# Optimization experiments

Measured on AMD Instinct MI355X. Metric: run time of the kernel, lower is better.

Reference implementation:

```python
import jax, jax.numpy as jnp
import numpy as np

M = 1024      # num_inducing
B = 131072    # batch of query points (original module is per-query; we vmap/vectorize)
EPS_D = 1e-8
JITTER = 1e-4

Z_SCALE = np.array([0.15, 0.1, 0.05, 800.0, 20.0], dtype=np.float32)
Z_SHIFT = np.array([0.0, 0.0, 0.0, 600.0, 5.0], dtype=np.float32)


def setup_inputs() -> dict:
    key = jax.random.key(0)
    k1, k2 = jax.random.split(key)
    x_star = jax.random.normal(k1, (B, 5), dtype=jnp.float32)
    # learnable params, sized/initialized per the flax module
    log_lengthscale = jnp.log(jnp.array([0.2, 0.15, 0.1, 400.0, 15.0], dtype=jnp.float32))
    log_variance = jnp.asarray(jnp.log(0.08), dtype=jnp.float32)
    Z_raw = jax.random.uniform(k2, (M, 5), dtype=jnp.float32)  # uniform(scale=1.0) init
    return {"x_star": x_star, "log_lengthscale": log_lengthscale,
            "log_variance": log_variance, "Z_raw": Z_raw}


def _pairwise_sqdist(A, Bm):
    # ||a-b||^2 via gemm; A:(n,d), Bm:(m,d) -> (n,m)
    aa = jnp.sum(A * A, axis=-1)
    bb = jnp.sum(Bm * Bm, axis=-1)
    d2 = aa[:, None] + bb[None, :] - 2.0 * (A @ Bm.T)
    return jnp.maximum(d2, 0.0)


def _matern52(d2, prior_var):
    d = jnp.sqrt(d2 + EPS_D)
    s = jnp.sqrt(5.0) * d
    return prior_var * (1.0 + s + (5.0 / 3.0) * (d * d)) * jnp.exp(-s)


def reference(x_star, log_lengthscale, log_variance, Z_raw):
    ls = jnp.exp(log_lengthscale)                # (5,)
    prior_var = jnp.exp(log_variance)            # scalar
    Z = Z_raw * jnp.asarray(Z_SCALE) + jnp.asarray(Z_SHIFT)  # (M,5)
    inv_ls = 1.0 / (ls + 1e-8)
    Zs = Z * inv_ls                              # lengthscale-scaled inducing pts
    Xs = x_star * inv_ls                         # (B,5)

    K_ZZ = _matern52(_pairwise_sqdist(Zs, Zs), prior_var)            # (M,M)
    K_ZZ_inv = jnp.linalg.inv(K_ZZ + JITTER * jnp.eye(M, dtype=K_ZZ.dtype))

    k_xZ = _matern52(_pairwise_sqdist(Xs, Zs), prior_var)            # (B,M)
    red = jnp.sum(k_xZ * (k_xZ @ K_ZZ_inv), axis=-1)                 # (B,)
    variance = jnp.maximum(prior_var - red, 1e-6)
    return jnp.sqrt(variance)                                        # (B,) predictive std
```

## Files before the change

kernel.cpp:

```cpp
#include <hip/hip_runtime.h>
#include <math.h>

#define B_TOT 131072
#define M_N   1024
#define BS    128
#define NBK   8

typedef float  f32x4  __attribute__((ext_vector_type(4)));
typedef short  bf16x8 __attribute__((ext_vector_type(8)));

enum : size_t {
    OFF_K   = 0,
    OFF_WF  = (size_t)8 << 20,
    OFF_W11 = (size_t)12 << 20,
    OFF_PF  = (size_t)13 << 20,
    OFF_ZT  = ((size_t)13 << 20) + 256,
    OFF_WPH = (size_t)14 << 20,
    OFF_WPL = (size_t)16 << 20,
};

__device__ __constant__ double c_zscale[5] = {0.15, 0.1, 0.05, 800.0, 20.0};
__device__ __constant__ double c_zshift[5] = {0.0, 0.0, 0.0, 600.0, 5.0};

static __device__ __forceinline__ unsigned short f2bf(float f) {
    unsigned u = __float_as_uint(f);
    unsigned r = (u + 0x7fff + ((u >> 16) & 1)) >> 16;
    return (unsigned short)r;
}
static __device__ __forceinline__ float bf2f(unsigned short s) {
    return __uint_as_float(((unsigned)s) << 16);
}

__global__ __launch_bounds__(256) void k_build(const float* __restrict__ log_ls,
                                               const float* __restrict__ log_var,
                                               const float* __restrict__ Zraw,
                                               double* __restrict__ Kd,
                                               float* __restrict__ pf,
                                               float* __restrict__ Zst) {
    __shared__ double pd[6];
    __shared__ double zsi[5];
    int tid = threadIdx.x;
    if (tid < 5) pd[tid] = 1.0 / (exp((double)log_ls[tid]) + 1e-8);
    if (tid == 5) pd[5] = exp((double)log_var[0]);
    __syncthreads();
    int i = blockIdx.x >> 2;
    int j = (blockIdx.x & 3) * 256 + tid;
    if (tid < 5) zsi[tid] = ((double)Zraw[i * 5 + tid] * c_zscale[tid] + c_zshift[tid]) * pd[tid];
    __syncthreads();
    double d2 = 0.0;
#pragma unroll
    for (int d = 0; d < 5; ++d) {
        double zj = ((double)Zraw[j * 5 + d] * c_zscale[d] + c_zshift[d]) * pd[d];
        double df = zsi[d] - zj;
        d2 += df * df;
    }
    double dd = d2 + 1e-8;
    double dist = sqrt(dd);
    double s = 2.2360679774997896 * dist;
    double v = pd[5] * (1.0 + s + (5.0 / 3.0) * dd) * exp(-s);
    if (i == j) v += 1e-4;
    Kd[(size_t)i * M_N + j] = v;
    if (blockIdx.x < 4) {
        int m = blockIdx.x * 256 + tid;
#pragma unroll
        for (int d = 0; d < 5; ++d)
            Zst[d * M_N + m] = (float)(((double)Zraw[m * 5 + d] * c_zscale[d] + c_zshift[d]) * pd[d]);
    }
    if (blockIdx.x == 4 && tid < 6) pf[tid] = (float)pd[tid];
}

__global__ __launch_bounds__(512) void kw_diag(double* __restrict__ Kd,
                                               double* __restrict__ Wd11,
                                               float* __restrict__ Wf, int kb) {
    __shared__ double As[128][129];
    __shared__ double sinv[128];
    int tid = threadIdx.x;
    int r0 = kb * BS;
    for (int idx = tid; idx < BS * BS; idx += 512) {
        int rr = idx >> 7, cc = idx & 127;
        As[rr][cc] = Kd[(size_t)(r0 + rr) * M_N + r0 + cc];
    }
    __syncthreads();

    int r = tid & 127;
    int q = tid >> 7;
    for (int p = 0; p < 16; ++p) {
        int j0 = p * 8;
        for (int j = j0; j < j0 + 8; ++j) {
            if (tid == j) {
                double d = sqrt(As[j][j]);
                As[j][j] = d;
                sinv[j] = 1.0 / d;
            }
            __syncthreads();
            double arj = 0.0;
            if (q == 0 && r > j) {
                arj = As[r][j] * sinv[j];
                As[r][j] = arj;
            }
            __syncthreads();
            if (q == 0 && r > j) {
#pragma unroll
                for (int c = j + 1; c < j0 + 8; ++c)
                    As[r][c] -= arj * As[c][j];
            }
        }
        __syncthreads();
        if (p < 15) {
            double a[8];
#pragma unroll
            for (int t = 0; t < 8; ++t) a[t] = As[r][j0 + t];
            for (int c = j0 + 8 + q; c < 128; c += 4) {
                if (r >= c) {
                    double s = As[r][c];
#pragma unroll
                    for (int t = 0; t < 8; ++t) s -= a[t] * As[c][j0 + t];
                    As[r][c] = s;
                }
            }
        }
        __syncthreads();
    }

    if (tid < 128) {
        int c = tid;
        for (int rb = 0; rb < 16; ++rb) {
            int r0b = rb * 8;
            if (c >= r0b + 8) continue;
            double s[8];
#pragma unroll
            for (int i = 0; i < 8; ++i) s[i] = 0.0;
            for (int t = 0; t < r0b; ++t) {
                if (t >= c) {
                    double xt = (t == c) ? sinv[c] : As[c][t];
#pragma unroll
                    for (int i = 0; i < 8; ++i) s[i] += As[r0b + i][t] * xt;
                }
            }
            double xloc[8];
#pragma unroll
            for (int i = 0; i < 8; ++i) {
                int rr = r0b + i;
                double v = 0.0;
                if (rr >= c) {
                    v = ((rr == c) ? 1.0 : 0.0) - s[i];
#pragma unroll
                    for (int t2 = 0; t2 < i; ++t2) {
                        int tt = r0b + t2;
                        if (tt >= c) v -= As[rr][tt] * xloc[t2];
                    }
                    v *= sinv[rr];
                    if (rr > c) As[c][rr] = v;
                }
                xloc[i] = v;
            }
        }
    }
    __syncthreads();
    for (int idx = tid; idx < BS * BS; idx += 512) {
        int rr = idx >> 7, cc = idx & 127;
        if (rr >= cc) {
            double v = (rr == cc) ? sinv[rr] : As[cc][rr];
            Wd11[(size_t)kb * BS * BS + rr * BS + cc] = v;
            Wf[(size_t)(r0 + rr) * M_N + r0 + cc] = (float)v;
        }
    }
}

__global__ __launch_bounds__(256) void kw_panel(double* __restrict__ Kd,
                                                const double* __restrict__ Wd11, int kb) {
    __shared__ double As[64][16];
    __shared__ double Ws[16][128];
    int tid = threadIdx.x;
    int row0 = (kb + 1) * BS + blockIdx.x * 64;
    int cb = kb * BS;
    int c = tid & 127, q = tid >> 7;
    double acc[32];
#pragma unroll
    for (int i = 0; i < 32; ++i) acc[i] = 0.0;
    for (int tc = 0; tc < 8; ++tc) {
        int tb = tc * 16;
        for (int idx = tid; idx < 64 * 16; idx += 256) {
            int rr = idx >> 4, tt = idx & 15;
            As[rr][tt] = Kd[(size_t)(row0 + rr) * M_N + cb + tb + tt];
        }
        for (int idx = tid; idx < 128 * 16; idx += 256) {
            int cc = idx >> 4, tt = idx & 15;
            Ws[tt][cc] = (tb + tt <= cc) ? Wd11[(size_t)kb * BS * BS + cc * BS + tb + tt] : 0.0;
        }
        __syncthreads();
#pragma unroll
        for (int t = 0; t < 16; ++t) {
            double w = Ws[t][c];
#pragma unroll
            for (int i = 0; i < 32; ++i) acc[i] += As[q * 32 + i][t] * w;
        }
        __syncthreads();
    }
#pragma unroll
    for (int i = 0; i < 32; ++i)
        Kd[(size_t)(row0 + q * 32 + i) * M_N + cb + c] = acc[i];
}

__global__ __launch_bounds__(256) void kw_update(double* __restrict__ Kd, int kb) {
    __shared__ double As2[64][17];
    __shared__ double Bs2[64][17];
    int tid = threadIdx.x;
    int v = blockIdx.x;
    int by = 0;
    while ((by + 1) * (by + 2) / 2 <= v) ++by;
    int bx = v - by * (by + 1) / 2;
    int base = (kb + 1) * BS;
    int gr0 = base + by * 64;
    int gc0 = base + bx * 64;
    int cb = kb * BS;
    int tx = tid & 15, ty = tid >> 4;
    double acc[4][4];
#pragma unroll
    for (int i = 0; i < 4; ++i)
#pragma unroll
        for (int j = 0; j < 4; ++j) acc[i][j] = 0.0;
    for (int tc = 0; tc < 8; ++tc) {
        int tb = tc * 16;
        for (int idx = tid; idx < 1024; idx += 256) {
            int rr = idx >> 4, tt = idx & 15;
            As2[rr][tt] = Kd[(size_t)(gr0 + rr) * M_N + cb + tb + tt];
            Bs2[rr][tt] = Kd[(size_t)(gc0 + rr) * M_N + cb + tb + tt];
        }
        __syncthreads();
#pragma unroll
        for (int t = 0; t < 16; ++t) {
            double a[4], b[4];
#pragma unroll
            for (int i = 0; i < 4; ++i) a[i] = As2[ty * 4 + i][t];
#pragma unroll
            for (int j = 0; j < 4; ++j) b[j] = Bs2[tx * 4 + j][t];
#pragma unroll
            for (int i = 0; i < 4; ++i)
#pragma unroll
                for (int j = 0; j < 4; ++j) acc[i][j] += a[i] * b[j];
        }
        __syncthreads();
    }
#pragma unroll
    for (int i = 0; i < 4; ++i)
#pragma unroll
        for (int j = 0; j < 4; ++j)
            Kd[(size_t)(gr0 + ty * 4 + i) * M_N + gc0 + tx * 4 + j] -= acc[i][j];
}

__global__ __launch_bounds__(512) void kw_trtri(const double* __restrict__ Kd,
                                                float* __restrict__ Wf) {
    __shared__ float Ls[128][33];
    __shared__ float Ws[32][33];
    __shared__ float Whist[6][128][33];
    __shared__ float Ps[128][33];
    int j  = blockIdx.y;
    int ct = blockIdx.x;
    int c0 = j * BS + ct * 32;
    int tid = threadIdx.x;
    int rq = tid >> 2, cq = tid & 3;

    for (int i = j + 1; i < 8; ++i) {
        float acc[8];
#pragma unroll
        for (int c = 0; c < 8; ++c) acc[c] = 0.0f;
        for (int t = j; t < i; ++t) {
            for (int ch = 0; ch < 4; ++ch) {
                int tb = t * BS + ch * 32;
                __syncthreads();
                for (int idx = tid; idx < 128 * 32; idx += 512) {
                    int rr = idx >> 5, tt = idx & 31;
                    Ls[rr][tt] = (float)Kd[(size_t)(i * BS + rr) * M_N + tb + tt];
                }
                if (t == j) {
                    for (int idx = tid; idx < 32 * 32; idx += 512) {
                        int tt = idx >> 5, cc = idx & 31;
                        int gr = tb + tt, gc = c0 + cc;
                        Ws[tt][cc] = (gr >= gc) ? Wf[(size_t)gr * M_N + gc] : 0.0f;
                    }
                }
                __syncthreads();
                if (t == j) {
#pragma unroll
                    for (int tt = 0; tt < 32; ++tt) {
                        float l = Ls[rq][tt];
#pragma unroll
                        for (int c = 0; c < 8; ++c)
                            acc[c] = fmaf(l, Ws[tt][cq * 8 + c], acc[c]);
                    }
                } else {
                    const float (*Wh)[33] = Whist[t - j - 1];
#pragma unroll
                    for (int tt = 0; tt < 32; ++tt) {
                        float l = Ls[rq][tt];
#pragma unroll
                        for (int c = 0; c < 8; ++c)
                            acc[c] = fmaf(l, Wh[ch * 32 + tt][cq * 8 + c], acc[c]);
                    }
                }
            }
        }
        __syncthreads();
#pragma unroll
        for (int c = 0; c < 8; ++c) Ps[rq][cq * 8 + c] = acc[c];
        float a2[8];
#pragma unroll
        for (int c = 0; c < 8; ++c) a2[c] = 0.0f;
        for (int ch = 0; ch < 4; ++ch) {
            __syncthreads();
            for (int idx = tid; idx < 128 * 32; idx += 512) {
                int rr = idx >> 5, tt = idx & 31;
                Ls[rr][tt] = (rr >= ch * 32 + tt)
                           ? Wf[(size_t)(i * BS + rr) * M_N + i * BS + ch * 32 + tt] : 0.0f;
            }
            __syncthreads();
#pragma unroll
            for (int tt = 0; tt < 32; ++tt) {
                float l = Ls[rq][tt];
#pragma unroll
                for (int c = 0; c < 8; ++c)
                    a2[c] = fmaf(l, Ps[ch * 32 + tt][cq * 8 + c], a2[c]);
            }
        }
        __syncthreads();
#pragma unroll
        for (int c = 0; c < 8; ++c) {
            float v = -a2[c];
            Wf[(size_t)(i * BS + rq) * M_N + c0 + cq * 8 + c] = v;
            if (i < 7) Whist[i - j - 1][rq][cq * 8 + c] = v;
        }
        __syncthreads();
    }
}

__global__ void kw_pack(const float* __restrict__ Wf, short* __restrict__ Wph,
                        short* __restrict__ Wpl) {
    int T = blockIdx.x * 256 + threadIdx.x;
    int lane = T & 63, fid = T >> 6;
    int jn = fid & 63, kik = fid >> 6;
    int ki = kik & 3, kc = kik >> 2;
    int j  = jn * 16 + (lane & 15);
    int kb = kc * 128 + ki * 32 + (lane >> 4) * 8;
    bf16x8 h, lo;
#pragma unroll
    for (int e = 0; e < 8; ++e) {
        int k = kb + e;
        float v = (k <= j) ? Wf[(size_t)j * M_N + k] : 0.0f;
        unsigned short hb = f2bf(v);
        h[e]  = (short)hb;
        lo[e] = (short)f2bf(v - bf2f(hb));
    }
    size_t off = (size_t)fid * 512 + lane * 8;
    *(bf16x8*)(Wph + off) = h;
    *(bf16x8*)(Wpl + off) = lo;
}

__global__ __launch_bounds__(512, 1) void k_mm(const float* __restrict__ x_star,
                                               const float* __restrict__ pf,
                                               const float* __restrict__ Zs_t,
                                               const short* __restrict__ Wph,
                                               const short* __restrict__ Wpl,
                                               float* __restrict__ out, int Bq) {
    __shared__ __align__(16) char kls[2][32 * 256];
    __shared__ float red_l[32];
    int tid  = threadIdx.x;
    int slab = blockIdx.x;
    int w = tid >> 6, lane = tid & 63;
    int lrow = lane & 15, kgrp = lane >> 4;

    int srow = tid >> 4, scc = tid & 15;
    int qrow = slab * 32 + srow;
    int qc = (qrow < Bq) ? qrow : (Bq - 1);
    float xv0 = x_star[(size_t)qc * 5 + 0] * pf[0];
    float xv1 = x_star[(size_t)qc * 5 + 1] * pf[1];
    float xv2 = x_star[(size_t)qc * 5 + 2] * pf[2];
    float xv3 = x_star[(size_t)qc * 5 + 3] * pf[3];
    float xv4 = x_star[(size_t)qc * 5 + 4] * pf[4];
    float pv = pf[5];
    if (tid < 32) red_l[tid] = 0.0f;

    f32x4 acc[2][8];
#pragma unroll
    for (int mi = 0; mi < 2; ++mi)
#pragma unroll
        for (int nj = 0; nj < 8; ++nj) acc[mi][nj] = (f32x4)(0.0f);

    int jmax_w = (56 + ((w + 7) & 7)) * 16 + 15;
    int soff = srow * 256 + ((scc * 16) ^ ((srow & 15) << 4));

    for (int kc = 0; kc < 8; ++kc) {
        int lb = kc * 128 + scc * 8;
        float kv[8];
#pragma unroll
        for (int h = 0; h < 2; ++h) {
            float z0[4], z1[4], z2[4], z3[4], z4[4];
            *(float4*)z0 = *(const float4*)&Zs_t[lb + 4 * h];
            *(float4*)z1 = *(const float4*)&Zs_t[M_N + lb + 4 * h];
            *(float4*)z2 = *(const float4*)&Zs_t[2 * M_N + lb + 4 * h];
            *(float4*)z3 = *(const float4*)&Zs_t[3 * M_N + lb + 4 * h];
            *(float4*)z4 = *(const float4*)&Zs_t[4 * M_N + lb + 4 * h];
#pragma unroll
            for (int e = 0; e < 4; ++e) {
                float dx0 = xv0 - z0[e], dx1 = xv1 - z1[e], dx2 = xv2 - z2[e],
                      dx3 = xv3 - z3[e], dx4 = xv4 - z4[e];
                float d2 = dx0 * dx0 + dx1 * dx1 + dx2 * dx2 + dx3 * dx3 + dx4 * dx4;
                float ddv = d2 + 1e-8f;
                float dist = sqrtf(ddv);
                float sv = 2.23606798f * dist;
                kv[h * 4 + e] = pv * (1.0f + sv + 1.66666667f * ddv) * __expf(-sv);
            }
        }
        bf16x8 hv, lv;
#pragma unroll
        for (int e = 0; e < 8; ++e) {
            unsigned short hb = f2bf(kv[e]);
            hv[e] = (short)hb;
            lv[e] = (short)f2bf(kv[e] - bf2f(hb));
        }
        __syncthreads();
        *(bf16x8*)(&kls[0][soff]) = hv;
        *(bf16x8*)(&kls[1][soff]) = lv;
        __syncthreads();

        for (int ki = 0; ki < 4; ++ki) {
            int kmin = kc * 128 + ki * 32;
            if (kmin > jmax_w) break;
            bf16x8 Ah[2], Al[2];
#pragma unroll
            for (int mi = 0; mi < 2; ++mi) {
                int row = mi * 16 + lrow;
                int cb  = ki * 64 + kgrp * 16;
                int off = row * 256 + (cb ^ ((row & 15) << 4));
                Ah[mi] = *(const bf16x8*)(&kls[0][off]);
                Al[mi] = *(const bf16x8*)(&kls[1][off]);
            }
#pragma unroll
            for (int nj = 0; nj < 8; ++nj) {
                int jng = nj * 8 + ((w + nj) & 7);
                if (kmin > jng * 16 + 15) continue;
                size_t fo = ((size_t)((kc * 4 + ki) * 64 + jng)) * 512 + lane * 8;
                bf16x8 Bh = *(const bf16x8*)(Wph + fo);
                bf16x8 Bl = *(const bf16x8*)(Wpl + fo);
#pragma unroll
                for (int mi = 0; mi < 2; ++mi) {
                    acc[mi][nj] = __builtin_amdgcn_mfma_f32_16x16x32_bf16(Ah[mi], Bh, acc[mi][nj], 0, 0, 0);
                    acc[mi][nj] = __builtin_amdgcn_mfma_f32_16x16x32_bf16(Ah[mi], Bl, acc[mi][nj], 0, 0, 0);
                    acc[mi][nj] = __builtin_amdgcn_mfma_f32_16x16x32_bf16(Al[mi], Bh, acc[mi][nj], 0, 0, 0);
                }
            }
        }
    }

#pragma unroll
    for (int mi = 0; mi < 2; ++mi) {
#pragma unroll
        for (int q = 0; q < 4; ++q) {
            float s = 0.0f;
#pragma unroll
            for (int nj = 0; nj < 8; ++nj) s = fmaf(acc[mi][nj][q], acc[mi][nj][q], s);
            s += __shfl_xor(s, 1);
            s += __shfl_xor(s, 2);
            s += __shfl_xor(s, 4);
            s += __shfl_xor(s, 8);
            if (lrow == 0) atomicAdd(&red_l[mi * 16 + kgrp * 4 + q], s);
        }
    }
    __syncthreads();
    if (tid < 32) {
        int b = slab * 32 + tid;
        if (b < Bq) out[b] = sqrtf(fmaxf(pv - red_l[tid], 1e-6f));
    }
}

extern "C" void kernel_launch(void* const* d_in, const int* in_sizes, int n_in,
                              void* d_out, int out_size, void* d_ws, size_t ws_size,
                              hipStream_t stream) {
    const float* x_star  = (const float*)d_in[0];
    const float* log_ls  = (const float*)d_in[1];
    const float* log_var = (const float*)d_in[2];
    const float* Z_raw   = (const float*)d_in[3];
    float* out = (float*)d_out;
    int Bq = in_sizes[0] / 5;

    char* ws = (char*)d_ws;
    double* Kd   = (double*)(ws + OFF_K);
    float*  Wf   = (float*)(ws + OFF_WF);
    double* Wd11 = (double*)(ws + OFF_W11);
    float*  pf   = (float*)(ws + OFF_PF);
    float*  Zst  = (float*)(ws + OFF_ZT);
    short*  Wph  = (short*)(ws + OFF_WPH);
    short*  Wpl  = (short*)(ws + OFF_WPL);

    k_build<<<4096, 256, 0, stream>>>(log_ls, log_var, Z_raw, Kd, pf, Zst);

    for (int kb = 0; kb < NBK; ++kb) {
        kw_diag<<<1, 512, 0, stream>>>(Kd, Wd11, Wf, kb);
        int R = M_N - (kb + 1) * BS;
        if (R > 0) {
            int nt = R / 64;
            kw_panel<<<nt, 256, 0, stream>>>(Kd, Wd11, kb);
            kw_update<<<nt * (nt + 1) / 2, 256, 0, stream>>>(Kd, kb);
        }
    }
    kw_trtri<<<dim3(4, 7), 512, 0, stream>>>(Kd, Wf);
    kw_pack<<<512, 256, 0, stream>>>(Wf, Wph, Wpl);

    int slabs = (Bq + 31) / 32;
    k_mm<<<slabs, 512, 0, stream>>>(x_star, pf, Zst, Wph, Wpl, out, Bq);
}
```

Before: 3.727 ms.

## Switch Cholesky to fp32, fuse panel+update, use fp16 two-term MFMA, split N

Moves the whole K_ZZ factorization pipeline from fp64 to fp32 and fuses the panel solve into the trailing update kernel, which recomputes the panel strips per tile and writes L from the diagonal tiles. The main batched product now uses fp16 instead of bf16, with the activation kept as a single fp16 term and the weight split into hi/lo, so it issues two MFMAs per tile instead of three. The output columns are split across two grid halves with 256-thread blocks, and partial reductions are summed by a new finalize kernel. Dropping fp64 and one MFMA term lowers the work, but it risks accuracy loss in inverting a jittered, possibly ill-conditioned matrix, and fp16 range or precision limits on the kernel values. Panel work is also duplicated across update tiles.

```diff
diff --git a/kernel.cpp b/kernel.cpp
--- a/kernel.cpp
+++ b/kernel.cpp
@@ -6,94 +6,84 @@
 #define BS    128
 #define NBK   8
 
-typedef float  f32x4  __attribute__((ext_vector_type(4)));
-typedef short  bf16x8 __attribute__((ext_vector_type(8)));
+typedef float    f32x4 __attribute__((ext_vector_type(4)));
+typedef _Float16 f16x8 __attribute__((ext_vector_type(8)));
 
 enum : size_t {
-    OFF_K   = 0,
+    OFF_KF  = 0,
+    OFF_LF  = (size_t)4 << 20,
     OFF_WF  = (size_t)8 << 20,
-    OFF_W11 = (size_t)12 << 20,
-    OFF_PF  = (size_t)13 << 20,
-    OFF_ZT  = ((size_t)13 << 20) + 256,
-    OFF_WPH = (size_t)14 << 20,
-    OFF_WPL = (size_t)16 << 20,
+    OFF_WPH = (size_t)12 << 20,
+    OFF_WPL = (size_t)14 << 20,
+    OFF_RED = (size_t)16 << 20,
+    OFF_PF  = (size_t)17 << 20,
+    OFF_ZT  = ((size_t)17 << 20) + 256,
 };
 
-__device__ __constant__ double c_zscale[5] = {0.15, 0.1, 0.05, 800.0, 20.0};
-__device__ __constant__ double c_zshift[5] = {0.0, 0.0, 0.0, 600.0, 5.0};
-
-static __device__ __forceinline__ unsigned short f2bf(float f) {
-    unsigned u = __float_as_uint(f);
-    unsigned r = (u + 0x7fff + ((u >> 16) & 1)) >> 16;
-    return (unsigned short)r;
-}
-static __device__ __forceinline__ float bf2f(unsigned short s) {
-    return __uint_as_float(((unsigned)s) << 16);
-}
+__device__ __constant__ float c_zscale[5] = {0.15f, 0.1f, 0.05f, 800.0f, 20.0f};
+__device__ __constant__ float c_zshift[5] = {0.0f, 0.0f, 0.0f, 600.0f, 5.0f};
 
 __global__ __launch_bounds__(256) void k_build(const float* __restrict__ log_ls,
                                                const float* __restrict__ log_var,
                                                const float* __restrict__ Zraw,
-                                               double* __restrict__ Kd,
+                                               float* __restrict__ Kf,
                                                float* __restrict__ pf,
                                                float* __restrict__ Zst) {
-    __shared__ double pd[6];
-    __shared__ double zsi[5];
+    __shared__ float ps[6];
+    __shared__ float zsi[5];
     int tid = threadIdx.x;
-    if (tid < 5) pd[tid] = 1.0 / (exp((double)log_ls[tid]) + 1e-8);
-    if (tid == 5) pd[5] = exp((double)log_var[0]);
+    if (tid < 5) ps[tid] = 1.0f / (__expf(log_ls[tid]) + 1e-8f);
+    if (tid == 5) ps[5] = __expf(log_var[0]);
     __syncthreads();
     int i = blockIdx.x >> 2;
     int j = (blockIdx.x & 3) * 256 + tid;
-    if (tid < 5) zsi[tid] = ((double)Zraw[i * 5 + tid] * c_zscale[tid] + c_zshift[tid]) * pd[tid];
+    if (tid < 5) zsi[tid] = (Zraw[i * 5 + tid] * c_zscale[tid] + c_zshift[tid]) * ps[tid];
     __syncthreads();
-    double d2 = 0.0;
+    float d2 = 0.0f;
 #pragma unroll
     for (int d = 0; d < 5; ++d) {
-        double zj = ((double)Zraw[j * 5 + d] * c_zscale[d] + c_zshift[d]) * pd[d];
-        double df = zsi[d] - zj;
+        float zj = (Zraw[j * 5 + d] * c_zscale[d] + c_zshift[d]) * ps[d];
+        float df = zsi[d] - zj;
         d2 += df * df;
     }
-    double dd = d2 + 1e-8;
-    double dist = sqrt(dd);
-    double s = 2.2360679774997896 * dist;
-    double v = pd[5] * (1.0 + s + (5.0 / 3.0) * dd) * exp(-s);
-    if (i == j) v += 1e-4;
-    Kd[(size_t)i * M_N + j] = v;
+    float dd = d2 + 1e-8f;
+    float dist = sqrtf(dd);
+    float s = 2.23606798f * dist;
+    float v = ps[5] * (1.0f + s + 1.66666667f * dd) * __expf(-s);
+    if (i == j) v += 1e-4f;
+    Kf[(size_t)i * M_N + j] = v;
     if (blockIdx.x < 4) {
         int m = blockIdx.x * 256 + tid;
 #pragma unroll
         for (int d = 0; d < 5; ++d)
-            Zst[d * M_N + m] = (float)(((double)Zraw[m * 5 + d] * c_zscale[d] + c_zshift[d]) * pd[d]);
-    }
-    if (blockIdx.x == 4 && tid < 6) pf[tid] = (float)pd[tid];
-}
-
-__global__ __launch_bounds__(512) void kw_diag(double* __restrict__ Kd,
-                                               double* __restrict__ Wd11,
+            Zst[d * M_N + m] = (Zraw[m * 5 + d] * c_zscale[d] + c_zshift[d]) * ps[d];
+    }
+    if (blockIdx.x == 4 && tid < 6) pf[tid] = ps[tid];
+}
+
+__global__ __launch_bounds__(512) void kw_diag(float* __restrict__ Kf,
                                                float* __restrict__ Wf, int kb) {
-    __shared__ double As[128][129];
-    __shared__ double sinv[128];
+    __shared__ float As[128][129];
+    __shared__ float sinv[128];
     int tid = threadIdx.x;
     int r0 = kb * BS;
     for (int idx = tid; idx < BS * BS; idx += 512) {
         int rr = idx >> 7, cc = idx & 127;
-        As[rr][cc] = Kd[(size_t)(r0 + rr) * M_N + r0 + cc];
+        As[rr][cc] = Kf[(size_t)(r0 + rr) * M_N + r0 + cc];
     }
     __syncthreads();
 
-    int r = tid & 127;
-    int q = tid >> 7;
+    int r = tid & 127, q = tid >> 7;
     for (int p = 0; p < 16; ++p) {
         int j0 = p * 8;
         for (int j = j0; j < j0 + 8; ++j) {
             if (tid == j) {
-                double d = sqrt(As[j][j]);
+                float d = sqrtf(As[j][j]);
                 As[j][j] = d;
-                sinv[j] = 1.0 / d;
+                sinv[j] = 1.0f / d;
             }
             __syncthreads();
-            double arj = 0.0;
+            float arj = 0.0f;
             if (q == 0 && r > j) {
                 arj = As[r][j] * sinv[j];
                 As[r][j] = arj;
@@ -107,12 +97,12 @@
         }
         __syncthreads();
         if (p < 15) {
-            double a[8];
+            float a[8];
 #pragma unroll
             for (int t = 0; t < 8; ++t) a[t] = As[r][j0 + t];
             for (int c = j0 + 8 + q; c < 128; c += 4) {
                 if (r >= c) {
-                    double s = As[r][c];
+                    float s = As[r][c];
 #pragma unroll
                     for (int t = 0; t < 8; ++t) s -= a[t] * As[c][j0 + t];
                     As[r][c] = s;
@@ -127,23 +117,23 @@
         for (int rb = 0; rb < 16; ++rb) {
             int r0b = rb * 8;
             if (c >= r0b + 8) continue;
-            double s[8];
-#pragma unroll
-            for (int i = 0; i < 8; ++i) s[i] = 0.0;
+            float s[8];
+#pragma unroll
+            for (int i = 0; i < 8; ++i) s[i] = 0.0f;
             for (int t = 0; t < r0b; ++t) {
                 if (t >= c) {
-                    double xt = (t == c) ? sinv[c] : As[c][t];
+                    float xt = (t == c) ? sinv[c] : As[c][t];
 #pragma unroll
                     for (int i = 0; i < 8; ++i) s[i] += As[r0b + i][t] * xt;
                 }
             }
-            double xloc[8];
+            float xloc[8];
 #pragma unroll
             for (int i = 0; i < 8; ++i) {
                 int rr = r0b + i;
-                double v = 0.0;
+                float v = 0.0f;
                 if (rr >= c) {
-                    v = ((rr == c) ? 1.0 : 0.0) - s[i];
+                    v = ((rr == c) ? 1.0f : 0.0f) - s[i];
 #pragma unroll
                     for (int t2 = 0; t2 < i; ++t2) {
                         int tt = r0b + t2;
@@ -159,97 +149,92 @@
     __syncthreads();
     for (int idx = tid; idx < BS * BS; idx += 512) {
         int rr = idx >> 7, cc = idx & 127;
-        if (rr >= cc) {
-            double v = (rr == cc) ? sinv[rr] : As[cc][rr];
-            Wd11[(size_t)kb * BS * BS + rr * BS + cc] = v;
-            Wf[(size_t)(r0 + rr) * M_N + r0 + cc] = (float)v;
-        }
-    }
-}
-
-__global__ __launch_bounds__(256) void kw_panel(double* __restrict__ Kd,
-                                                const double* __restrict__ Wd11, int kb) {
-    __shared__ double As[64][16];
-    __shared__ double Ws[16][128];
-    int tid = threadIdx.x;
-    int row0 = (kb + 1) * BS + blockIdx.x * 64;
-    int cb = kb * BS;
+        if (rr >= cc)
+            Wf[(size_t)(r0 + rr) * M_N + r0 + cc] = (rr == cc) ? sinv[rr] : As[cc][rr];
+    }
+}
+
+static __device__ void d_strip(const float* __restrict__ Kf, const float* __restrict__ Wf,
+                               int cb, int row0, float (*S)[129],
+                               float (*Ast)[17], float (*Wst)[128], int tid) {
     int c = tid & 127, q = tid >> 7;
-    double acc[32];
-#pragma unroll
-    for (int i = 0; i < 32; ++i) acc[i] = 0.0;
+    float acc[32];
+#pragma unroll
+    for (int i = 0; i < 32; ++i) acc[i] = 0.0f;
     for (int tc = 0; tc < 8; ++tc) {
         int tb = tc * 16;
+        __syncthreads();
         for (int idx = tid; idx < 64 * 16; idx += 256) {
             int rr = idx >> 4, tt = idx & 15;
-            As[rr][tt] = Kd[(size_t)(row0 + rr) * M_N + cb + tb + tt];
+            Ast[rr][tt] = Kf[(size_t)(row0 + rr) * M_N + cb + tb + tt];
         }
         for (int idx = tid; idx < 128 * 16; idx += 256) {
             int cc = idx >> 4, tt = idx & 15;
-            Ws[tt][cc] = (tb + tt <= cc) ? Wd11[(size_t)kb * BS * BS + cc * BS + tb + tt] : 0.0;
+            Wst[tt][cc] = (tb + tt <= cc) ? Wf[(size_t)(cb + cc) * M_N + cb + tb + tt] : 0.0f;
         }
         __syncthreads();
 #pragma unroll
         for (int t = 0; t < 16; ++t) {
-            double w = Ws[t][c];
-#pragma unroll
-            for (int i = 0; i < 32; ++i) acc[i] += As[q * 32 + i][t] * w;
-        }
-        __syncthreads();
-    }
-#pragma unroll
-    for (int i = 0; i < 32; ++i)
-        Kd[(size_t)(row0 + q * 32 + i) * M_N + cb + c] = acc[i];
-}
-
-__global__ __launch_bounds__(256) void kw_update(double* __restrict__ Kd, int kb) {
-    __shared__ double As2[64][17];
-    __shared__ double Bs2[64][17];
+            float w = Wst[t][c];
+#pragma unroll
+            for (int i = 0; i < 32; ++i) acc[i] += Ast[q * 32 + i][t] * w;
+        }
+    }
+#pragma unroll
+    for (int i = 0; i < 32; ++i) S[q * 32 + i][c] = acc[i];
+}
+
+__global__ __launch_bounds__(256) void kw_step(float* __restrict__ Kf,
+                                               const float* __restrict__ Wf,
+                                               float* __restrict__ Lf, int kb) {
+    __shared__ float SA[64][129];
+    __shared__ float SB[64][129];
+    __shared__ float Ast[64][17];
+    __shared__ float Wst[16][128];
     int tid = threadIdx.x;
     int v = blockIdx.x;
     int by = 0;
     while ((by + 1) * (by + 2) / 2 <= v) ++by;
     int bx = v - by * (by + 1) / 2;
     int base = (kb + 1) * BS;
-    int gr0 = base + by * 64;
-    int gc0 = base + bx * 64;
     int cb = kb * BS;
+    int gr0 = base + by * 64, gc0 = base + bx * 64;
+
+    d_strip(Kf, Wf, cb, gr0, SA, Ast, Wst, tid);
+    if (bx != by) d_strip(Kf, Wf, cb, gc0, SB, Ast, Wst, tid);
+    float (*PB)[129] = (bx == by) ? SA : SB;
+    __syncthreads();
+
     int tx = tid & 15, ty = tid >> 4;
-    double acc[4][4];
+    float acc[4][4];
 #pragma unroll
     for (int i = 0; i < 4; ++i)
 #pragma unroll
-        for (int j = 0; j < 4; ++j) acc[i][j] = 0.0;
-    for (int tc = 0; tc < 8; ++tc) {
-        int tb = tc * 16;
-        for (int idx = tid; idx < 1024; idx += 256) {
-            int rr = idx >> 4, tt = idx & 15;
-            As2[rr][tt] = Kd[(size_t)(gr0 + rr) * M_N + cb + tb + tt];
-            Bs2[rr][tt] = Kd[(size_t)(gc0 + rr) * M_N + cb + tb + tt];
-        }
-        __syncthreads();
-#pragma unroll
-        for (int t = 0; t < 16; ++t) {
-            double a[4], b[4];
-#pragma unroll
-            for (int i = 0; i < 4; ++i) a[i] = As2[ty * 4 + i][t];
-#pragma unroll
-            for (int j = 0; j < 4; ++j) b[j] = Bs2[tx * 4 + j][t];
-#pragma unroll
-            for (int i = 0; i < 4; ++i)
-#pragma unroll
-                for (int j = 0; j < 4; ++j) acc[i][j] += a[i] * b[j];
-        }
-        __syncthreads();
+        for (int j = 0; j < 4; ++j) acc[i][j] = 0.0f;
+    for (int t = 0; t < 128; ++t) {
+        float a[4], b[4];
+#pragma unroll
+        for (int i = 0; i < 4; ++i) a[i] = SA[ty * 4 + i][t];
+#pragma unroll
+        for (int j = 0; j < 4; ++j) b[j] = PB[tx * 4 + j][t];
+#pragma unroll
+        for (int i = 0; i < 4; ++i)
+#pragma unroll
+            for (int j = 0; j < 4; ++j) acc[i][j] = fmaf(a[i], b[j], acc[i][j]);
     }
 #pragma unroll
     for (int i = 0; i < 4; ++i)
 #pragma unroll
         for (int j = 0; j < 4; ++j)
-            Kd[(size_t)(gr0 + ty * 4 + i) * M_N + gc0 + tx * 4 + j] -= acc[i][j];
-}
-
-__global__ __launch_bounds__(512) void kw_trtri(const double* __restrict__ Kd,
+            Kf[(size_t)(gr0 + ty * 4 + i) * M_N + gc0 + tx * 4 + j] -= acc[i][j];
+
+    if (by == bx) {
+        for (int idx = tid; idx < 64 * 128; idx += 256)
+            Lf[(size_t)(gr0 + (idx >> 7)) * M_N + cb + (idx & 127)] = SA[idx >> 7][idx & 127];
+    }
+}
+
+__global__ __launch_bounds__(512) void kw_trtri(const float* __restrict__ Lf,
                                                 float* __restrict__ Wf) {
     __shared__ float Ls[128][33];
     __shared__ float Ws[32][33];
@@ -271,7 +256,7 @@
                 __syncthreads();
                 for (int idx = tid; idx < 128 * 32; idx += 512) {
                     int rr = idx >> 5, tt = idx & 31;
-                    Ls[rr][tt] = (float)Kd[(size_t)(i * BS + rr) * M_N + tb + tt];
+                    Ls[rr][tt] = Lf[(size_t)(i * BS + rr) * M_N + tb + tt];
                 }
                 if (t == j) {
                     for (int idx = tid; idx < 32 * 32; idx += 512) {
@@ -334,42 +319,42 @@
     }
 }
 
-__global__ void kw_pack(const float* __restrict__ Wf, short* __restrict__ Wph,
-                        short* __restrict__ Wpl) {
+__global__ void kw_pack(const float* __restrict__ Wf, _Float16* __restrict__ Wph,
+                        _Float16* __restrict__ Wpl) {
     int T = blockIdx.x * 256 + threadIdx.x;
     int lane = T & 63, fid = T >> 6;
     int jn = fid & 63, kik = fid >> 6;
     int ki = kik & 3, kc = kik >> 2;
     int j  = jn * 16 + (lane & 15);
     int kb = kc * 128 + ki * 32 + (lane >> 4) * 8;
-    bf16x8 h, lo;
+    f16x8 h, lo;
 #pragma unroll
     for (int e = 0; e < 8; ++e) {
         int k = kb + e;
         float v = (k <= j) ? Wf[(size_t)j * M_N + k] : 0.0f;
-        unsigned short hb = f2bf(v);
-        h[e]  = (short)hb;
-        lo[e] = (short)f2bf(v - bf2f(hb));
+        _Float16 hh = (_Float16)v;
+        h[e]  = hh;
+        lo[e] = (_Float16)(v - (float)hh);
     }
     size_t off = (size_t)fid * 512 + lane * 8;
-    *(bf16x8*)(Wph + off) = h;
-    *(bf16x8*)(Wpl + off) = lo;
-}
-
-__global__ __launch_bounds__(512, 1) void k_mm(const float* __restrict__ x_star,
-                                               const float* __restrict__ pf,
-                                               const float* __restrict__ Zs_t,
-                                               const short* __restrict__ Wph,
-                                               const short* __restrict__ Wpl,
-                                               float* __restrict__ out, int Bq) {
-    __shared__ __align__(16) char kls[2][32 * 256];
+    *(f16x8*)(Wph + off) = h;
+    *(f16x8*)(Wpl + off) = lo;
+}
+
+__global__ __launch_bounds__(256) void k_mm(const float* __restrict__ x_star,
+                                            const float* __restrict__ pf,
+                                            const float* __restrict__ Zst,
+                                            const _Float16* __restrict__ Wph,
+                                            const _Float16* __restrict__ Wpl,
+                                            float* __restrict__ redp, int Bq) {
+    __shared__ __align__(16) char kls[32 * 256];
     __shared__ float red_l[32];
     int tid  = threadIdx.x;
-    int slab = blockIdx.x;
+    int slab = blockIdx.x, pp = blockIdx.y;
     int w = tid >> 6, lane = tid & 63;
     int lrow = lane & 15, kgrp = lane >> 4;
 
-    int srow = tid >> 4, scc = tid & 15;
+    int srow = tid >> 3, sg = tid & 7;
     int qrow = slab * 32 + srow;
     int qc = (qrow < Bq) ? qrow : (Bq - 1);
     float xv0 = x_star[(size_t)qc * 5 + 0] * pf[0];
@@ -386,67 +371,66 @@
 #pragma unroll
         for (int nj = 0; nj < 8; ++nj) acc[mi][nj] = (f32x4)(0.0f);
 
-    int jmax_w = (56 + ((w + 7) & 7)) * 16 + 15;
-    int soff = srow * 256 + ((scc * 16) ^ ((srow & 15) << 4));
-
-    for (int kc = 0; kc < 8; ++kc) {
-        int lb = kc * 128 + scc * 8;
-        float kv[8];
-#pragma unroll
-        for (int h = 0; h < 2; ++h) {
-            float z0[4], z1[4], z2[4], z3[4], z4[4];
-            *(float4*)z0 = *(const float4*)&Zs_t[lb + 4 * h];
-            *(float4*)z1 = *(const float4*)&Zs_t[M_N + lb + 4 * h];
-            *(float4*)z2 = *(const float4*)&Zs_t[2 * M_N + lb + 4 * h];
-            *(float4*)z3 = *(const float4*)&Zs_t[3 * M_N + lb + 4 * h];
-            *(float4*)z4 = *(const float4*)&Zs_t[4 * M_N + lb + 4 * h];
-#pragma unroll
-            for (int e = 0; e < 4; ++e) {
+    int jmax_w = (pp * 32 + 28 + ((w + 3) & 3)) * 16 + 15;
+    int KC = pp ? 8 : 4;
+
+    for (int kc = 0; kc < KC; ++kc) {
+        f16x8 hv[2];
+#pragma unroll
+        for (int b = 0; b < 2; ++b) {
+            int lb = kc * 128 + sg * 16 + b * 8;
+            float z0[8], z1[8], z2[8], z3[8], z4[8];
+            *(float4*)&z0[0] = *(const float4*)&Zst[lb];
+            *(float4*)&z0[4] = *(const float4*)&Zst[lb + 4];
+            *(float4*)&z1[0] = *(const float4*)&Zst[M_N + lb];
+            *(float4*)&z1[4] = *(const float4*)&Zst[M_N + lb + 4];
+            *(float4*)&z2[0] = *(const float4*)&Zst[2 * M_N + lb];
+            *(float4*)&z2[4] = *(const float4*)&Zst[2 * M_N + lb + 4];
+            *(float4*)&z3[0] = *(const float4*)&Zst[3 * M_N + lb];
+            *(float4*)&z3[4] = *(const float4*)&Zst[3 * M_N + lb + 4];
+            *(float4*)&z4[0] = *(const float4*)&Zst[4 * M_N + lb];
+            *(float4*)&z4[4] = *(const float4*)&Zst[4 * M_N + lb + 4];
+#pragma unroll
+            for (int e = 0; e < 8; ++e) {
                 float dx0 = xv0 - z0[e], dx1 = xv1 - z1[e], dx2 = xv2 - z2[e],
                       dx3 = xv3 - z3[e], dx4 = xv4 - z4[e];
                 float d2 = dx0 * dx0 + dx1 * dx1 + dx2 * dx2 + dx3 * dx3 + dx4 * dx4;
                 float ddv = d2 + 1e-8f;
                 float dist = sqrtf(ddv);
                 float sv = 2.23606798f * dist;
-                kv[h * 4 + e] = pv * (1.0f + sv + 1.66666667f * ddv) * __expf(-sv);
-            }
-        }
-        bf16x8 hv, lv;
-#pragma unroll
-        for (int e = 0; e < 8; ++e) {
-            unsigned short hb = f2bf(kv[e]);
-            hv[e] = (short)hb;
-            lv[e] = (short)f2bf(kv[e] - bf2f(hb));
-        }
-        __syncthreads();
-        *(bf16x8*)(&kls[0][soff]) = hv;
-        *(bf16x8*)(&kls[1][soff]) = lv;
+                hv[b][e] = (_Float16)(pv * (1.0f + sv + 1.66666667f * ddv) * __expf(-sv));
+            }
+        }
+        __syncthreads();
+        {
+            int o0 = srow * 256 + ((sg * 32) ^ ((srow & 15) << 4));
+            int o1 = srow * 256 + ((sg * 32 + 16) ^ ((srow & 15) << 4));
+            *(f16x8*)(&kls[o0]) = hv[0];
+            *(f16x8*)(&kls[o1]) = hv[1];
+        }
         __syncthreads();
 
         for (int ki = 0; ki < 4; ++ki) {
             int kmin = kc * 128 + ki * 32;
             if (kmin > jmax_w) break;
-            bf16x8 Ah[2], Al[2];
+            f16x8 A_[2];
 #pragma unroll
             for (int mi = 0; mi < 2; ++mi) {
                 int row = mi * 16 + lrow;
                 int cb  = ki * 64 + kgrp * 16;
-                int off = row * 256 + (cb ^ ((row & 15) << 4));
-                Ah[mi] = *(const bf16x8*)(&kls[0][off]);
-                Al[mi] = *(const bf16x8*)(&kls[1][off]);
+                A_[mi] = *(const f16x8*)(&kls[row * 256 + (cb ^ ((row & 15) << 4))]);
             }
 #pragma unroll
             for (int nj = 0; nj < 8; ++nj) {
-                int jng = nj * 8 + ((w + nj) & 7);
+                int jng = pp * 32 + nj * 4 + ((w + nj) & 3);
                 if (kmin > jng * 16 + 15) continue;
                 size_t fo = ((size_t)((kc * 4 + ki) * 64 + jng)) * 512 + lane * 8;
-                bf16x8 Bh = *(const bf16x8*)(Wph + fo);
-                bf16x8 Bl = *(const bf16x8*)(Wpl + fo);
+                f16x8 Bh = *(const f16x8*)(Wph + fo);
+                f16x8 Bl = *(const f16x8*)(Wpl + fo);
 #pragma unroll
                 for (int mi = 0; mi < 2; ++mi) {
-                    acc[mi][nj] = __builtin_amdgcn_mfma_f32_16x16x32_bf16(Ah[mi], Bh, acc[mi][nj], 0, 0, 0);
-                    acc[mi][nj] = __builtin_amdgcn_mfma_f32_16x16x32_bf16(Ah[mi], Bl, acc[mi][nj], 0, 0, 0);
-                    acc[mi][nj] = __builtin_amdgcn_mfma_f32_16x16x32_bf16(Al[mi], Bh, acc[mi][nj], 0, 0, 0);
+                    acc[mi][nj] = __builtin_amdgcn_mfma_f32_16x16x32_f16(A_[mi], Bh, acc[mi][nj], 0, 0, 0);
+                    acc[mi][nj] = __builtin_amdgcn_mfma_f32_16x16x32_f16(A_[mi], Bl, acc[mi][nj], 0, 0, 0);
                 }
             }
         }
@@ -469,7 +453,16 @@
     __syncthreads();
     if (tid < 32) {
         int b = slab * 32 + tid;
-        if (b < Bq) out[b] = sqrtf(fmaxf(pv - red_l[tid], 1e-6f));
+        if (b < Bq) redp[(size_t)pp * Bq + b] = red_l[tid];
+    }
+}
+
+__global__ void k_fin(const float* __restrict__ redp, const float* __restrict__ pf,
+                      float* __restrict__ out, int Bq) {
+    int b = blockIdx.x * 256 + threadIdx.x;
+    if (b < Bq) {
+        float red = redp[b] + redp[(size_t)Bq + b];
+        out[b] = sqrtf(fmaxf(pf[5] - red, 1e-6f));
     }
 }
 
@@ -484,28 +477,29 @@
     int Bq = in_sizes[0] / 5;
 
     char* ws = (char*)d_ws;
-    double* Kd   = (double*)(ws + OFF_K);
-    float*  Wf   = (float*)(ws + OFF_WF);
-    double* Wd11 = (double*)(ws + OFF_W11);
-    float*  pf   = (float*)(ws + OFF_PF);
-    float*  Zst  = (float*)(ws + OFF_ZT);
-    short*  Wph  = (short*)(ws + OFF_WPH);
-    short*  Wpl  = (short*)(ws + OFF_WPL);
-
-    k_build<<<4096, 256, 0, stream>>>(log_ls, log_var, Z_raw, Kd, pf, Zst);
+    float*     Kf   = (float*)(ws + OFF_KF);
+    float*     Lf   = (float*)(ws + OFF_LF);
+    float*     Wf   = (float*)(ws + OFF_WF);
+    _Float16*  Wph  = (_Float16*)(ws + OFF_WPH);
+    _Float16*  Wpl  = (_Float16*)(ws + OFF_WPL);
+    float*     redp = (float*)(ws + OFF_RED);
+    float*     pf   = (float*)(ws + OFF_PF);
+    float*     Zst  = (float*)(ws + OFF_ZT);
+
+    k_build<<<4096, 256, 0, stream>>>(log_ls, log_var, Z_raw, Kf, pf, Zst);
 
     for (int kb = 0; kb < NBK; ++kb) {
-        kw_diag<<<1, 512, 0, stream>>>(Kd, Wd11, Wf, kb);
+        kw_diag<<<1, 512, 0, stream>>>(Kf, Wf, kb);
         int R = M_N - (kb + 1) * BS;
         if (R > 0) {
             int nt = R / 64;
-            kw_panel<<<nt, 256, 0, stream>>>(Kd, Wd11, kb);
-            kw_update<<<nt * (nt + 1) / 2, 256, 0, stream>>>(Kd, kb);
-        }
-    }
-    kw_trtri<<<dim3(4, 7), 512, 0, stream>>>(Kd, Wf);
+            kw_step<<<nt * (nt + 1) / 2, 256, 0, stream>>>(Kf, Wf, Lf, kb);
+        }
+    }
+    kw_trtri<<<dim3(4, 7), 512, 0, stream>>>(Lf, Wf);
     kw_pack<<<512, 256, 0, stream>>>(Wf, Wph, Wpl);
 
     int slabs = (Bq + 31) / 32;
-    k_mm<<<slabs, 512, 0, stream>>>(x_star, pf, Zst, Wph, Wpl, out, Bq);
-}
+    k_mm<<<dim3(slabs, 2), 256, 0, stream>>>(x_star, pf, Zst, Wph, Wpl, redp, Bq);
+    k_fin<<<(Bq + 255) / 256, 256, 0, stream>>>(redp, pf, out, Bq);
+}
```

Result: faster. 3.555 ms (-4.6%).
